# Performance work log

Hardware: AMD Instinct MI355X
Metric: run time of the kernel (lower is better)

Reference implementation:

```python
import jax, jax.numpy as jnp
import numpy as np

K = 10  # knn neighbors
GF = 100  # gf_num = 25*4


def setup_inputs() -> dict:
    key = jax.random.key(0)
    ks = jax.random.split(key, 14)
    B, N = 4, 8192
    s = 0.1
    inp = {
        "x": jax.random.normal(ks[0], (B, N, 3), dtype=jnp.float32),
        # conv1: (3+K)->20->GF, 1x1 convs == per-point linears
        "w1a": jax.random.normal(ks[1], (3 + K, 20), jnp.float32) * s,
        "b1a": jax.random.normal(ks[2], (20,), jnp.float32) * s,
        "w1b": jax.random.normal(ks[3], (20, GF), jnp.float32) * s,
        "b1b": jax.random.normal(ks[4], (GF,), jnp.float32) * s,
        # conv2: GF->GF
        "w2": jax.random.normal(ks[5], (GF, GF), jnp.float32) * s,
        "b2": jax.random.normal(ks[6], (GF,), jnp.float32) * s,
        # conv3: 2*GF->20->10->2
        "w3a": jax.random.normal(ks[7], (2 * GF, 20), jnp.float32) * s,
        "b3a": jax.random.normal(ks[8], (20,), jnp.float32) * s,
        "w3b": jax.random.normal(ks[9], (20, 10), jnp.float32) * s,
        "b3b": jax.random.normal(ks[10], (10,), jnp.float32) * s,
        "w3c": jax.random.normal(ks[11], (10, 2), jnp.float32) * s,
        "b3c": jax.random.normal(ks[12], (2,), jnp.float32) * s,
    }
    return inp


def reference(x, w1a, b1a, w1b, b1b, w2, b2, w3a, b3a, w3b, b3b, w3c, b3c):
    # pairwise squared distances: [B, N, N]
    sq = jnp.sum(x * x, axis=-1)
    d = sq[:, :, None] + sq[:, None, :] - 2.0 * jnp.einsum("bnc,bmc->bnm", x, x)
    # k smallest distances per point, ascending order (matches torch topk largest=False)
    topk = -jax.lax.top_k(-d, K)[0]  # [B, N, K]
    h = jnp.concatenate([x, topk], axis=-1)  # [B, N, 3+K]
    # conv1 (1x1 convs == per-point linears)
    x1 = jax.nn.relu(jax.nn.relu(h @ w1a + b1a) @ w1b + b1b)  # [B, N, GF]
    # conv2
    x2 = jax.nn.relu(x1 @ w2 + b2)  # [B, N, GF]
    # global avg pool over points, broadcast back
    pool = jnp.mean(x2, axis=1, keepdims=True)  # [B, 1, GF]
    N = x1.shape[1]
    feat = jnp.concatenate([x1, jnp.broadcast_to(pool, (x1.shape[0], N, pool.shape[-1]))], axis=-1)
    # conv3 head + log-softmax over the 2 classes (torch dim=-2 on [B,2,N] layout)
    o = jax.nn.relu(feat @ w3a + b3a)
    o = jax.nn.relu(o @ w3b + b3b)
    o = o @ w3c + b3c  # [B, N, 2]
    return jax.nn.log_softmax(o, axis=-1)
```

## Files before the change

### kernel.cpp

```cpp
#include <hip/hip_runtime.h>
#include <math.h>

#define N_PTS   8192
#define NBATCH  4
#define NQ      (N_PTS*NBATCH)
#define GFN     100
#define KNN     10
#define NSPLIT  8
#define SPLITL  (N_PTS/NSPLIT)
#define PTS_BLK 64
#define CH      13

__device__ __forceinline__ float med3f(float a, float b, float c){
  return __builtin_amdgcn_fmed3f(a, b, c);
}

__device__ __forceinline__ void insert10(float (&m)[KNN], float d){
  #pragma unroll
  for (int k = KNN-1; k > 0; k--) m[k] = med3f(d, m[k-1], m[k]);
  m[0] = fminf(m[0], d);
}

__global__ __launch_bounds__(256) void knn_kernel(const float* __restrict__ x,
                                                  float* __restrict__ cand,
                                                  float* __restrict__ pool){
  __shared__ float4 tile[SPLITL];
  const int t  = threadIdx.x;
  const int qb = blockIdx.x;
  const int s  = blockIdx.y;
  const int q  = qb * 256 + t;
  const int b  = q >> 13;
  const float* xb = x + (size_t)b * N_PTS * 3;

  if (qb == 0 && s == 0){
    for (int i = t; i < NBATCH*GFN; i += 256) pool[i] = 0.0f;
  }

  #pragma unroll
  for (int k = 0; k < 4; k++){
    const int j = t + 256*k;
    const float* ps = xb + (size_t)(s*SPLITL + j)*3;
    float px = ps[0], py = ps[1], pz = ps[2];
    float sq = fmaf(pz, pz, fmaf(py, py, px*px));
    tile[j] = make_float4(px, py, pz, sq);
  }
  __syncthreads();

  const float xi = x[(size_t)q*3+0], yi = x[(size_t)q*3+1], zi = x[(size_t)q*3+2];
  const float sqi = fmaf(zi, zi, fmaf(yi, yi, xi*xi));

  float m[KNN];
  #pragma unroll
  for (int k = 0; k < KNN; k++) m[k] = INFINITY;

  #pragma unroll 8
  for (int j = 0; j < SPLITL; j++){
    float4 p = tile[j];
    float dot = fmaf(zi, p.z, fmaf(yi, p.y, xi*p.x));
    float d   = fmaf(-2.0f, dot, sqi + p.w);
    insert10(m, d);
  }

  #pragma unroll
  for (int k = 0; k < KNN; k++) cand[(size_t)(s*KNN + k)*NQ + q] = m[k];
}

__global__ __launch_bounds__(512) void mlp1_kernel(
    const float* __restrict__ x,   const float* __restrict__ cand,
    const float* __restrict__ w1a, const float* __restrict__ b1a,
    const float* __restrict__ w1b, const float* __restrict__ b1b,
    const float* __restrict__ w2,  const float* __restrict__ b2,
    float* __restrict__ x1t, float* __restrict__ pool){
  __shared__ float t20s[PTS_BLK*21];
  __shared__ float x1s[PTS_BLK*101];
  const int t = threadIdx.x;
  const int p = t & 63;
  const int g = __builtin_amdgcn_readfirstlane(t >> 6);
  const int q0 = blockIdx.x * PTS_BLK;
  const int q  = q0 + p;
  const int b  = q >> 13;

  if (g < 4){
    float m[KNN];
    #pragma unroll
    for (int k = 0; k < KNN; k++) m[k] = INFINITY;
    #pragma unroll
    for (int i = 0; i < NSPLIT*KNN; i++) insert10(m, cand[(size_t)i*NQ + q]);

    float h[13];
    h[0] = x[(size_t)q*3+0]; h[1] = x[(size_t)q*3+1]; h[2] = x[(size_t)q*3+2];
    #pragma unroll
    for (int k = 0; k < KNN; k++) h[3+k] = m[k];

    const float* wa = w1a + g*5;
    float a[5];
    #pragma unroll
    for (int j = 0; j < 5; j++) a[j] = b1a[g*5+j];
    #pragma unroll
    for (int c = 0; c < 13; c++){
      float hv = h[c];
      #pragma unroll
      for (int j = 0; j < 5; j++) a[j] = fmaf(hv, wa[c*20+j], a[j]);
    }
    #pragma unroll
    for (int j = 0; j < 5; j++) t20s[p*21 + g*5 + j] = fmaxf(a[j], 0.0f);
  }
  __syncthreads();

  float acc[CH];
  const int o0 = g * CH;

  {
    #pragma unroll
    for (int k = 0; k < CH; k++) acc[k] = (o0+k < GFN) ? b1b[o0+k] : 0.0f;
    #pragma unroll 4
    for (int c = 0; c < 20; c++){
      float tv = t20s[p*21 + c];
      #pragma unroll
      for (int k = 0; k < CH; k++)
        if (o0+k < GFN) acc[k] = fmaf(tv, w1b[c*GFN + o0+k], acc[k]);
    }
    #pragma unroll
    for (int k = 0; k < CH; k++){
      if (o0+k < GFN){
        float v = fmaxf(acc[k], 0.0f);
        x1s[p*101 + o0+k] = v;
        x1t[(size_t)(o0+k)*NQ + q] = v;
      }
    }
  }
  __syncthreads();

  {
    #pragma unroll
    for (int k = 0; k < CH; k++) acc[k] = (o0+k < GFN) ? b2[o0+k] : 0.0f;
    #pragma unroll 4
    for (int c = 0; c < GFN; c++){
      float xv = x1s[p*101 + c];
      #pragma unroll
      for (int k = 0; k < CH; k++)
        if (o0+k < GFN) acc[k] = fmaf(xv, w2[c*GFN + o0+k], acc[k]);
    }
    #pragma unroll
    for (int k = 0; k < CH; k++){
      if (o0+k < GFN){
        float v = fmaxf(acc[k], 0.0f);
        #pragma unroll
        for (int off = 1; off < 64; off <<= 1) v += __shfl_xor(v, off);
        if (p == 0) atomicAdd(&pool[b*GFN + o0+k], v);
      }
    }
  }
}

__global__ __launch_bounds__(128) void head_kernel(
    const float* __restrict__ x1t, const float* __restrict__ pool,
    const float* __restrict__ w3a, const float* __restrict__ b3a,
    const float* __restrict__ w3b, const float* __restrict__ b3b,
    const float* __restrict__ w3c, const float* __restrict__ b3c,
    float* __restrict__ out){
  __shared__ float poolm[GFN];
  __shared__ float poolpart[20];
  const int t = threadIdx.x;
  const int q = blockIdx.x * 128 + t;
  const int b = q >> 13;

  if (t < GFN) poolm[t] = pool[b*GFN+t] * (1.0f / (float)N_PTS);
  __syncthreads();
  if (t < 20){
    float a = b3a[t];
    for (int c = 0; c < GFN; c++) a = fmaf(poolm[c], w3a[(GFN+c)*20+t], a);
    poolpart[t] = a;
  }
  __syncthreads();

  float acc[20];
  #pragma unroll
  for (int o = 0; o < 20; o++) acc[o] = 0.0f;
  #pragma unroll 8
  for (int c = 0; c < GFN; c++){
    float xv = x1t[(size_t)c*NQ + q];
    #pragma unroll
    for (int o = 0; o < 20; o++) acc[o] = fmaf(xv, w3a[c*20+o], acc[o]);
  }
  float o1[20];
  #pragma unroll
  for (int o = 0; o < 20; o++) o1[o] = fmaxf(acc[o] + poolpart[o], 0.0f);

  float o2[10];
  #pragma unroll
  for (int o = 0; o < 10; o++){
    float a = b3b[o];
    #pragma unroll
    for (int c = 0; c < 20; c++) a = fmaf(o1[c], w3b[c*10+o], a);
    o2[o] = fmaxf(a, 0.0f);
  }
  float e0 = b3c[0], e1 = b3c[1];
  #pragma unroll
  for (int c = 0; c < 10; c++){
    e0 = fmaf(o2[c], w3c[c*2+0], e0);
    e1 = fmaf(o2[c], w3c[c*2+1], e1);
  }
  float mx = fmaxf(e0, e1);
  float a0 = e0 - mx, a1 = e1 - mx;
  float lse = logf(expf(a0) + expf(a1));
  float2 r; r.x = a0 - lse; r.y = a1 - lse;
  *reinterpret_cast<float2*>(out + (size_t)q*2) = r;
}

extern "C" void kernel_launch(void* const* d_in, const int* in_sizes, int n_in,
                              void* d_out, int out_size, void* d_ws, size_t ws_size,
                              hipStream_t stream) {
  const float* x   = (const float*)d_in[0];
  const float* w1a = (const float*)d_in[1];
  const float* b1a = (const float*)d_in[2];
  const float* w1b = (const float*)d_in[3];
  const float* b1b = (const float*)d_in[4];
  const float* w2  = (const float*)d_in[5];
  const float* b2  = (const float*)d_in[6];
  const float* w3a = (const float*)d_in[7];
  const float* b3a = (const float*)d_in[8];
  const float* w3b = (const float*)d_in[9];
  const float* b3b = (const float*)d_in[10];
  const float* w3c = (const float*)d_in[11];
  const float* b3c = (const float*)d_in[12];
  float* out = (float*)d_out;

  char* ws = (char*)d_ws;
  float* cand = (float*)ws;
  float* x1t  = (float*)(ws + (size_t)NQ*NSPLIT*KNN*4);
  float* pool = (float*)(ws + (size_t)NQ*NSPLIT*KNN*4
                            + (size_t)GFN*NQ*4);

  knn_kernel<<<dim3(NQ/256, NSPLIT), 256, 0, stream>>>(x, cand, pool);
  mlp1_kernel<<<NQ/PTS_BLK, 512, 0, stream>>>(x, cand, w1a, b1a, w1b, b1b, w2, b2, x1t, pool);
  head_kernel<<<NQ/128, 128, 0, stream>>>(x1t, pool, w3a, b3a, w3b, b3b, w3c, b3c, out);
}
```

Before: 322.6 us.

## Register-tile MLP kernel over two points per thread with 25-channel slices

The per-point MLP kernel now handles 128 points per 256-thread block. Each wave computes 25 output channels for two points at once, so every weight load feeds two FMAs. The first layer is computed by two waves, each producing all 20 hidden outputs for its point instead of splitting them across four waves. This aims to cut weight-load and LDS traffic and to remove the wasted channel padding of the old 13-channel split. In exchange it raises register pressure and halves the number of active waves per point block, which may lower occupancy.

```diff
diff --git a/kernel.cpp b/kernel.cpp
--- a/kernel.cpp
+++ b/kernel.cpp
@@ -8,8 +8,8 @@
 #define KNN     10
 #define NSPLIT  8
 #define SPLITL  (N_PTS/NSPLIT)
-#define PTS_BLK 64
-#define CH      13
+#define MBLK    128
+#define CHK     25
 
 __device__ __forceinline__ float med3f(float a, float b, float c){
   return __builtin_amdgcn_fmed3f(a, b, c);
@@ -65,22 +65,23 @@
   for (int k = 0; k < KNN; k++) cand[(size_t)(s*KNN + k)*NQ + q] = m[k];
 }
 
-__global__ __launch_bounds__(512) void mlp1_kernel(
+__global__ __launch_bounds__(256) void mlp1_kernel(
     const float* __restrict__ x,   const float* __restrict__ cand,
     const float* __restrict__ w1a, const float* __restrict__ b1a,
     const float* __restrict__ w1b, const float* __restrict__ b1b,
     const float* __restrict__ w2,  const float* __restrict__ b2,
     float* __restrict__ x1t, float* __restrict__ pool){
-  __shared__ float t20s[PTS_BLK*21];
-  __shared__ float x1s[PTS_BLK*101];
+  __shared__ float t20s[MBLK*21];
+  __shared__ float x1s[MBLK*101];
   const int t = threadIdx.x;
   const int p = t & 63;
   const int g = __builtin_amdgcn_readfirstlane(t >> 6);
-  const int q0 = blockIdx.x * PTS_BLK;
-  const int q  = q0 + p;
-  const int b  = q >> 13;
-
-  if (g < 4){
+  const int q0 = blockIdx.x * MBLK;
+  const int b  = q0 >> 13;
+
+  if (g < 2){
+    const int pr = g*64 + p;
+    const int q  = q0 + pr;
     float m[KNN];
     #pragma unroll
     for (int k = 0; k < KNN; k++) m[k] = INFINITY;
@@ -92,63 +93,72 @@
     #pragma unroll
     for (int k = 0; k < KNN; k++) h[3+k] = m[k];
 
-    const float* wa = w1a + g*5;
-    float a[5];
-    #pragma unroll
-    for (int j = 0; j < 5; j++) a[j] = b1a[g*5+j];
+    float a[20];
+    #pragma unroll
+    for (int o = 0; o < 20; o++) a[o] = b1a[o];
     #pragma unroll
     for (int c = 0; c < 13; c++){
       float hv = h[c];
       #pragma unroll
-      for (int j = 0; j < 5; j++) a[j] = fmaf(hv, wa[c*20+j], a[j]);
-    }
-    #pragma unroll
-    for (int j = 0; j < 5; j++) t20s[p*21 + g*5 + j] = fmaxf(a[j], 0.0f);
-  }
-  __syncthreads();
-
-  float acc[CH];
-  const int o0 = g * CH;
-
-  {
-    #pragma unroll
-    for (int k = 0; k < CH; k++) acc[k] = (o0+k < GFN) ? b1b[o0+k] : 0.0f;
-    #pragma unroll 4
-    for (int c = 0; c < 20; c++){
-      float tv = t20s[p*21 + c];
-      #pragma unroll
-      for (int k = 0; k < CH; k++)
-        if (o0+k < GFN) acc[k] = fmaf(tv, w1b[c*GFN + o0+k], acc[k]);
-    }
-    #pragma unroll
-    for (int k = 0; k < CH; k++){
-      if (o0+k < GFN){
-        float v = fmaxf(acc[k], 0.0f);
-        x1s[p*101 + o0+k] = v;
-        x1t[(size_t)(o0+k)*NQ + q] = v;
-      }
-    }
-  }
-  __syncthreads();
-
-  {
-    #pragma unroll
-    for (int k = 0; k < CH; k++) acc[k] = (o0+k < GFN) ? b2[o0+k] : 0.0f;
-    #pragma unroll 4
-    for (int c = 0; c < GFN; c++){
-      float xv = x1s[p*101 + c];
-      #pragma unroll
-      for (int k = 0; k < CH; k++)
-        if (o0+k < GFN) acc[k] = fmaf(xv, w2[c*GFN + o0+k], acc[k]);
-    }
-    #pragma unroll
-    for (int k = 0; k < CH; k++){
-      if (o0+k < GFN){
-        float v = fmaxf(acc[k], 0.0f);
-        #pragma unroll
-        for (int off = 1; off < 64; off <<= 1) v += __shfl_xor(v, off);
-        if (p == 0) atomicAdd(&pool[b*GFN + o0+k], v);
-      }
+      for (int o = 0; o < 20; o++) a[o] = fmaf(hv, w1a[c*20+o], a[o]);
+    }
+    #pragma unroll
+    for (int o = 0; o < 20; o++) t20s[pr*21 + o] = fmaxf(a[o], 0.0f);
+  }
+  __syncthreads();
+
+  const int o0 = g * CHK;
+  float accA[CHK], accB[CHK];
+
+  #pragma unroll
+  for (int k = 0; k < CHK; k++){ float bv = b1b[o0+k]; accA[k] = bv; accB[k] = bv; }
+  #pragma unroll 4
+  for (int c = 0; c < 20; c++){
+    float ta = t20s[p*21 + c];
+    float tb = t20s[(64+p)*21 + c];
+    #pragma unroll
+    for (int k = 0; k < CHK; k++){
+      float w = w1b[c*GFN + o0 + k];
+      accA[k] = fmaf(ta, w, accA[k]);
+      accB[k] = fmaf(tb, w, accB[k]);
+    }
+  }
+  #pragma unroll
+  for (int k = 0; k < CHK; k++){
+    float va = fmaxf(accA[k], 0.0f);
+    float vb = fmaxf(accB[k], 0.0f);
+    x1s[p*101 + o0 + k] = va;
+    x1s[(64+p)*101 + o0 + k] = vb;
+    x1t[(size_t)(o0+k)*NQ + q0 + p]      = va;
+    x1t[(size_t)(o0+k)*NQ + q0 + 64 + p] = vb;
+  }
+  __syncthreads();
+
+  #pragma unroll
+  for (int k = 0; k < CHK; k++){ float bv = b2[o0+k]; accA[k] = bv; accB[k] = bv; }
+  #pragma unroll 4
+  for (int c = 0; c < GFN; c++){
+    float xa = x1s[p*101 + c];
+    float xb = x1s[(64+p)*101 + c];
+    #pragma unroll
+    for (int k = 0; k < CHK; k++){
+      float w = w2[c*GFN + o0 + k];
+      accA[k] = fmaf(xa, w, accA[k]);
+      accB[k] = fmaf(xb, w, accB[k]);
+    }
+  }
+  #pragma unroll
+  for (int k = 0; k < CHK; k++){
+    float va = fmaxf(accA[k], 0.0f);
+    float vb = fmaxf(accB[k], 0.0f);
+    #pragma unroll
+    for (int off = 1; off < 64; off <<= 1){
+      va += __shfl_xor(va, off);
+      vb += __shfl_xor(vb, off);
+    }
+    if (p == 0){
+      atomicAdd(&pool[b*GFN + o0 + k], va);
+      atomicAdd(&pool[b*GFN + o0 + k], vb);
     }
   }
 }
@@ -233,6 +243,6 @@
                             + (size_t)GFN*NQ*4);
 
   knn_kernel<<<dim3(NQ/256, NSPLIT), 256, 0, stream>>>(x, cand, pool);
-  mlp1_kernel<<<NQ/PTS_BLK, 512, 0, stream>>>(x, cand, w1a, b1a, w1b, b1b, w2, b2, x1t, pool);
+  mlp1_kernel<<<NQ/MBLK, 256, 0, stream>>>(x, cand, w1a, b1a, w1b, b1b, w2, b2, x1t, pool);
   head_kernel<<<NQ/128, 128, 0, stream>>>(x1t, pool, w3a, b3a, w3b, b3b, w3c, b3c, out);
 }
```

Result: faster. 273.3 us (-15.3%).

## Add warp-uniform early-reject in kNN, reduce splits, vectorize tile load, widen MLP chunks

Applied to the files above, without the earlier changes.

The kNN scan now skips the 10-element insertion network when no lane in the wavefront has a distance below its current 10th-best, and it double-buffers tile reads in registers. The number of point splits drops from 8 to 2, so each block scans 4096 points held in a larger LDS tile loaded with float4 reads. This also cuts the candidate merge in the MLP kernel. The MLP kernel moves to 256 threads with 25 output channels per wave, removing the idle waves and bounds checks. The cost is fewer blocks (lower parallelism) and higher LDS use in the kNN kernel.

```diff
diff --git a/kernel.cpp b/kernel.cpp
--- a/kernel.cpp
+++ b/kernel.cpp
@@ -6,10 +6,10 @@
 #define NQ      (N_PTS*NBATCH)
 #define GFN     100
 #define KNN     10
-#define NSPLIT  8
+#define NSPLIT  2
 #define SPLITL  (N_PTS/NSPLIT)
-#define PTS_BLK 64
-#define CH      13
+#define MBLK    64
+#define CHK     25
 
 __device__ __forceinline__ float med3f(float a, float b, float c){
   return __builtin_amdgcn_fmed3f(a, b, c);
@@ -36,13 +36,20 @@
     for (int i = t; i < NBATCH*GFN; i += 256) pool[i] = 0.0f;
   }
 
-  #pragma unroll
-  for (int k = 0; k < 4; k++){
-    const int j = t + 256*k;
-    const float* ps = xb + (size_t)(s*SPLITL + j)*3;
-    float px = ps[0], py = ps[1], pz = ps[2];
-    float sq = fmaf(pz, pz, fmaf(py, py, px*px));
-    tile[j] = make_float4(px, py, pz, sq);
+  {
+    const float4* src = reinterpret_cast<const float4*>(xb + (size_t)s * SPLITL * 3);
+    float f[48];
+    #pragma unroll
+    for (int k = 0; k < 12; k++){
+      float4 v = src[t*12 + k];
+      f[4*k+0] = v.x; f[4*k+1] = v.y; f[4*k+2] = v.z; f[4*k+3] = v.w;
+    }
+    #pragma unroll
+    for (int p = 0; p < 16; p++){
+      float px = f[3*p+0], py = f[3*p+1], pz = f[3*p+2];
+      float sq = fmaf(pz, pz, fmaf(py, py, px*px));
+      tile[t*16 + p] = make_float4(px, py, pz, sq);
+    }
   }
   __syncthreads();
 
@@ -53,34 +60,46 @@
   #pragma unroll
   for (int k = 0; k < KNN; k++) m[k] = INFINITY;
 
-  #pragma unroll 8
-  for (int j = 0; j < SPLITL; j++){
-    float4 p = tile[j];
-    float dot = fmaf(zi, p.z, fmaf(yi, p.y, xi*p.x));
-    float d   = fmaf(-2.0f, dot, sqi + p.w);
-    insert10(m, d);
+  float4 buf[8];
+  #pragma unroll
+  for (int u = 0; u < 8; u++) buf[u] = tile[u];
+
+  for (int j0 = 0; j0 < SPLITL; j0 += 8){
+    float4 nxt[8];
+    const int jn = (j0+8 < SPLITL) ? (j0+8) : 0;
+    #pragma unroll
+    for (int u = 0; u < 8; u++) nxt[u] = tile[jn + u];
+    #pragma unroll
+    for (int u = 0; u < 8; u++){
+      float4 p = buf[u];
+      float dot = fmaf(zi, p.z, fmaf(yi, p.y, xi*p.x));
+      float d   = fmaf(-2.0f, dot, sqi + p.w);
+      if (__any(d < m[KNN-1])) insert10(m, d);
+    }
+    #pragma unroll
+    for (int u = 0; u < 8; u++) buf[u] = nxt[u];
   }
 
   #pragma unroll
   for (int k = 0; k < KNN; k++) cand[(size_t)(s*KNN + k)*NQ + q] = m[k];
 }
 
-__global__ __launch_bounds__(512) void mlp1_kernel(
+__global__ __launch_bounds__(256) void mlp1_kernel(
     const float* __restrict__ x,   const float* __restrict__ cand,
     const float* __restrict__ w1a, const float* __restrict__ b1a,
     const float* __restrict__ w1b, const float* __restrict__ b1b,
     const float* __restrict__ w2,  const float* __restrict__ b2,
     float* __restrict__ x1t, float* __restrict__ pool){
-  __shared__ float t20s[PTS_BLK*21];
-  __shared__ float x1s[PTS_BLK*101];
+  __shared__ float t20s[MBLK*21];
+  __shared__ float x1s[MBLK*101];
   const int t = threadIdx.x;
   const int p = t & 63;
   const int g = __builtin_amdgcn_readfirstlane(t >> 6);
-  const int q0 = blockIdx.x * PTS_BLK;
+  const int q0 = blockIdx.x * MBLK;
   const int q  = q0 + p;
-  const int b  = q >> 13;
-
-  if (g < 4){
+  const int b  = q0 >> 13;
+
+  {
     float m[KNN];
     #pragma unroll
     for (int k = 0; k < KNN; k++) m[k] = INFINITY;
@@ -92,7 +111,6 @@
     #pragma unroll
     for (int k = 0; k < KNN; k++) h[3+k] = m[k];
 
-    const float* wa = w1a + g*5;
     float a[5];
     #pragma unroll
     for (int j = 0; j < 5; j++) a[j] = b1a[g*5+j];
@@ -100,56 +118,46 @@
     for (int c = 0; c < 13; c++){
       float hv = h[c];
       #pragma unroll
-      for (int j = 0; j < 5; j++) a[j] = fmaf(hv, wa[c*20+j], a[j]);
+      for (int j = 0; j < 5; j++) a[j] = fmaf(hv, w1a[c*20 + g*5 + j], a[j]);
     }
     #pragma unroll
     for (int j = 0; j < 5; j++) t20s[p*21 + g*5 + j] = fmaxf(a[j], 0.0f);
   }
   __syncthreads();
 
-  float acc[CH];
-  const int o0 = g * CH;
-
-  {
-    #pragma unroll
-    for (int k = 0; k < CH; k++) acc[k] = (o0+k < GFN) ? b1b[o0+k] : 0.0f;
-    #pragma unroll 4
-    for (int c = 0; c < 20; c++){
-      float tv = t20s[p*21 + c];
-      #pragma unroll
-      for (int k = 0; k < CH; k++)
-        if (o0+k < GFN) acc[k] = fmaf(tv, w1b[c*GFN + o0+k], acc[k]);
-    }
-    #pragma unroll
-    for (int k = 0; k < CH; k++){
-      if (o0+k < GFN){
-        float v = fmaxf(acc[k], 0.0f);
-        x1s[p*101 + o0+k] = v;
-        x1t[(size_t)(o0+k)*NQ + q] = v;
-      }
-    }
-  }
-  __syncthreads();
-
-  {
-    #pragma unroll
-    for (int k = 0; k < CH; k++) acc[k] = (o0+k < GFN) ? b2[o0+k] : 0.0f;
-    #pragma unroll 4
-    for (int c = 0; c < GFN; c++){
-      float xv = x1s[p*101 + c];
-      #pragma unroll
-      for (int k = 0; k < CH; k++)
-        if (o0+k < GFN) acc[k] = fmaf(xv, w2[c*GFN + o0+k], acc[k]);
-    }
-    #pragma unroll
-    for (int k = 0; k < CH; k++){
-      if (o0+k < GFN){
-        float v = fmaxf(acc[k], 0.0f);
-        #pragma unroll
-        for (int off = 1; off < 64; off <<= 1) v += __shfl_xor(v, off);
-        if (p == 0) atomicAdd(&pool[b*GFN + o0+k], v);
-      }
-    }
+  const int o0 = g * CHK;
+  float acc[CHK];
+
+  #pragma unroll
+  for (int k = 0; k < CHK; k++) acc[k] = b1b[o0+k];
+  #pragma unroll 2
+  for (int c = 0; c < 20; c++){
+    float tv = t20s[p*21 + c];
+    #pragma unroll
+    for (int k = 0; k < CHK; k++) acc[k] = fmaf(tv, w1b[c*GFN + o0 + k], acc[k]);
+  }
+  #pragma unroll
+  for (int k = 0; k < CHK; k++){
+    float v = fmaxf(acc[k], 0.0f);
+    x1s[p*101 + o0 + k] = v;
+    x1t[(size_t)(o0+k)*NQ + q] = v;
+  }
+  __syncthreads();
+
+  #pragma unroll
+  for (int k = 0; k < CHK; k++) acc[k] = b2[o0+k];
+  #pragma unroll 2
+  for (int c = 0; c < GFN; c++){
+    float xv = x1s[p*101 + c];
+    #pragma unroll
+    for (int k = 0; k < CHK; k++) acc[k] = fmaf(xv, w2[c*GFN + o0 + k], acc[k]);
+  }
+  #pragma unroll
+  for (int k = 0; k < CHK; k++){
+    float v = fmaxf(acc[k], 0.0f);
+    #pragma unroll
+    for (int off = 1; off < 64; off <<= 1) v += __shfl_xor(v, off);
+    if (p == 0) atomicAdd(&pool[b*GFN + o0 + k], v);
   }
 }
 
@@ -233,6 +241,6 @@
                             + (size_t)GFN*NQ*4);
 
   knn_kernel<<<dim3(NQ/256, NSPLIT), 256, 0, stream>>>(x, cand, pool);
-  mlp1_kernel<<<NQ/PTS_BLK, 512, 0, stream>>>(x, cand, w1a, b1a, w1b, b1b, w2, b2, x1t, pool);
+  mlp1_kernel<<<NQ/MBLK, 256, 0, stream>>>(x, cand, w1a, b1a, w1b, b1b, w2, b2, x1t, pool);
   head_kernel<<<NQ/128, 128, 0, stream>>>(x1t, pool, w3a, b3a, w3b, b3b, w3c, b3c, out);
 }
```

Result: slower. 378.0 us (+17.2%).
